# Performance work log

Hardware: AMD Instinct MI355X
Metric: run time of the kernel (lower is better)

Reference implementation:

```python
import jax, jax.numpy as jnp
import numpy as np

DIM = 1024
N_HEADS = 16
HEAD_DIM = DIM // N_HEADS
B, T = 2, 2048


def get_rotary_embedding(T, head_dim, dtype=jnp.float32):
    inv_freq = 1.0 / (10000.0 ** (jnp.arange(0, head_dim, 2, dtype=jnp.float32) / head_dim))
    t = jnp.arange(T, dtype=jnp.float32)
    freqs = jnp.einsum('t,f->tf', t, inv_freq)          # [T, head_dim/2]
    emb = jnp.concatenate([freqs, freqs], axis=-1)       # [T, head_dim]
    return jnp.sin(emb).astype(dtype), jnp.cos(emb).astype(dtype)


def rotate_half(x):
    x1, x2 = jnp.split(x, 2, axis=-1)
    return jnp.concatenate([-x2, x1], axis=-1)


def apply_rotary_pos_emb(x, sin, cos):
    # x: [B, H, T, D]; sin/cos: [T, D] broadcast over B, H
    return x * cos + rotate_half(x) * sin


def setup_inputs() -> dict:
    key = jax.random.key(0)
    ks = jax.random.split(key, 4)
    s = DIM ** -0.5
    return {
        'x': jax.random.normal(ks[0], (B, T, DIM), jnp.float32),
        'W_qkv': jax.random.normal(ks[1], (DIM, 3 * DIM), jnp.float32) * s,
        'b_qkv': jnp.zeros((3 * DIM,), jnp.float32),
        'W_out': jax.random.normal(ks[2], (DIM, DIM), jnp.float32) * s,
        'b_out': jnp.zeros((DIM,), jnp.float32),
    }


def reference(x, W_qkv, b_qkv, W_out, b_out):
    Bc, Tc, C = x.shape
    scale = HEAD_DIM ** -0.5
    qkv = x @ W_qkv + b_qkv                                    # [B, T, 3C]
    qkv = qkv.reshape(Bc, Tc, 3, N_HEADS, HEAD_DIM)
    qkv = jnp.transpose(qkv, (2, 0, 3, 1, 4))                  # [3, B, H, T, D]
    q, k, v = qkv[0], qkv[1], qkv[2]
    sin, cos = get_rotary_embedding(Tc, HEAD_DIM, x.dtype)
    q = apply_rotary_pos_emb(q, sin, cos)
    k = apply_rotary_pos_emb(k, sin, cos)
    attn = jnp.einsum('bhqd,bhkd->bhqk', q, k) * scale         # [B, H, T, T]
    probs = jax.nn.softmax(attn, axis=-1)
    out = jnp.einsum('bhqk,bhkd->bhqd', probs, v)              # [B, H, T, D]
    out = jnp.transpose(out, (0, 2, 1, 3)).reshape(Bc, Tc, C)
    return out @ W_out + b_out
```

## Files before the change

### kernel.cpp

```cpp
#include <hip/hip_runtime.h>
#include <hip/hip_bf16.h>
#include <cstdint>
#include <cstddef>

typedef unsigned short ushort_t;
typedef __bf16 bf16x8 __attribute__((ext_vector_type(8)));
typedef float f32x4 __attribute__((ext_vector_type(4)));

#define DEV static __device__ __forceinline__

DEV void gl2lds16(const void* g, void* l) {
  __builtin_amdgcn_global_load_lds(
      (const __attribute__((address_space(1))) void*)(uintptr_t)g,
      (__attribute__((address_space(3))) void*)(uintptr_t)l, 16, 0, 0);
}

DEV bf16x8 ldfrag(const void* p) { return __builtin_bit_cast(bf16x8, *(const uint4*)p); }

DEV f32x4 mfma16(bf16x8 a, bf16x8 b, f32x4 c) {
  return __builtin_amdgcn_mfma_f32_16x16x32_bf16(a, b, c, 0, 0, 0);
}

DEV ushort_t f2b(float f) { return __builtin_bit_cast(ushort_t, __float2bfloat16(f)); }
DEV unsigned int cvtpk(float lo, float hi) {
  unsigned int r;
  asm("v_cvt_pk_bf16_f32 %0, %1, %2" : "=v"(r) : "v"(lo), "v"(hi));
  return r;
}

__global__ __launch_bounds__(256) void k_cast_bf16(const float* __restrict__ X,
                                                   ushort_t* __restrict__ Y, int n) {
  int i = (blockIdx.x * 256 + threadIdx.x) * 4;
  if (i >= n) return;
  float4 v = *(const float4*)(X + i);
  ushort4 o;
  o.x = f2b(v.x); o.y = f2b(v.y); o.z = f2b(v.z); o.w = f2b(v.w);
  *(ushort4*)(Y + i) = o;
}

__global__ __launch_bounds__(256) void k_castT(const float* __restrict__ W,
                                               ushort_t* __restrict__ WT, int K, int N) {
  __shared__ ushort_t tile[64][72];
  int n0 = blockIdx.x * 64, k0 = blockIdx.y * 64;
  int t = threadIdx.x;
#pragma unroll
  for (int i = 0; i < 16; ++i) {
    int e = i * 256 + t; int r = e >> 6, c = e & 63;
    tile[c][r] = f2b(W[(size_t)(k0 + r) * N + n0 + c]);
  }
  __syncthreads();
#pragma unroll
  for (int i = 0; i < 16; ++i) {
    int e = i * 256 + t; int rn = e >> 6, ck = e & 63;
    WT[(size_t)(n0 + rn) * K + k0 + ck] = tile[rn][ck];
  }
}

__global__ __launch_bounds__(256) void k_rope_table(float* __restrict__ sintab,
                                                    float* __restrict__ costab) {
  int id = blockIdx.x * 256 + threadIdx.x;
  int f = id & 31, t = id >> 5;
  float invf = exp2f(-(float)f * 0.4152410118609203f);
  float ang = (float)t * invf;
  sintab[id] = sinf(ang);
  costab[id] = cosf(ang);
}

template <int EPI, int BM, int BN>
__global__ __launch_bounds__(256, 2) void k_gemm_bt(
    const ushort_t* __restrict__ A, const ushort_t* __restrict__ BT,
    const float* __restrict__ bias, ushort_t* __restrict__ Oq,
    ushort_t* __restrict__ Ok, ushort_t* __restrict__ Ov,
    float* __restrict__ Of, const float* __restrict__ sintab,
    const float* __restrict__ costab, int K, int N) {
  constexpr int MI = BM / 32, NJ = BN / 32;
  __shared__ __align__(16) char As[2][BM * 64];
  __shared__ __align__(16) char Bs[2][BN * 64];
  const int tid = threadIdx.x, lane = tid & 63, wv = tid >> 6;
  const int l15 = lane & 15, l4 = lane >> 4;
  const int nt = blockIdx.x, mt = blockIdx.y;
  const char* Ab = (const char*)(A + (size_t)mt * BM * K);
  const char* Bb = (const char*)(BT + (size_t)nt * BN * K);
  const int rs = K * 2;
  const int wr = (wv >> 1) * (BM / 2), wc = (wv & 1) * (BN / 2);
  f32x4 acc[MI][NJ] = {};
#pragma unroll
  for (int ii = 0; ii < BM / 64; ++ii) {
    int slot = wv * (BM / 64) + ii;
    int r = slot * 16 + (lane >> 2);
    int scb = ((lane & 3) * 16) ^ ((r & 3) << 4);
    gl2lds16(Ab + (size_t)r * rs + scb, As[0] + slot * 1024);
  }
#pragma unroll
  for (int ii = 0; ii < BN / 64; ++ii) {
    int slot = wv * (BN / 64) + ii;
    int r = slot * 16 + (lane >> 2);
    int scb = ((lane & 3) * 16) ^ ((r & 3) << 4);
    gl2lds16(Bb + (size_t)r * rs + scb, Bs[0] + slot * 1024);
  }
  __syncthreads();
  for (int k0 = 0; k0 < K; k0 += 32) {
    const int cur = (k0 >> 5) & 1;
    if (k0 + 32 < K) {
#pragma unroll
      for (int ii = 0; ii < BM / 64; ++ii) {
        int slot = wv * (BM / 64) + ii;
        int r = slot * 16 + (lane >> 2);
        int scb = ((lane & 3) * 16) ^ ((r & 3) << 4);
        gl2lds16(Ab + (size_t)r * rs + (k0 + 32) * 2 + scb, As[cur ^ 1] + slot * 1024);
      }
#pragma unroll
      for (int ii = 0; ii < BN / 64; ++ii) {
        int slot = wv * (BN / 64) + ii;
        int r = slot * 16 + (lane >> 2);
        int scb = ((lane & 3) * 16) ^ ((r & 3) << 4);
        gl2lds16(Bb + (size_t)r * rs + (k0 + 32) * 2 + scb, Bs[cur ^ 1] + slot * 1024);
      }
    }
    bf16x8 af[MI], bg[NJ];
#pragma unroll
    for (int i = 0; i < MI; ++i) {
      int r = wr + i * 16 + l15;
      af[i] = ldfrag(As[cur] + r * 64 + ((l4 * 16) ^ ((r & 3) << 4)));
    }
#pragma unroll
    for (int j = 0; j < NJ; ++j) {
      int r = wc + j * 16 + l15;
      bg[j] = ldfrag(Bs[cur] + r * 64 + ((l4 * 16) ^ ((r & 3) << 4)));
    }
    __builtin_amdgcn_s_setprio(1);
#pragma unroll
    for (int i = 0; i < MI; ++i)
#pragma unroll
      for (int j = 0; j < NJ; ++j)
        acc[i][j] = mfma16(af[i], bg[j], acc[i][j]);
    __builtin_amdgcn_s_setprio(0);
    __syncthreads();
  }
  if constexpr (EPI == 0) {
    const int colbase = nt * BN + wc;
    const int part = colbase >> 10;
    const int h = (colbase >> 6) & 15;
    float bv[NJ];
#pragma unroll
    for (int j = 0; j < NJ; ++j) bv[j] = bias[colbase + j * 16 + l15];
    if (part <= 1) {
      ushort_t* dst = part ? Ok : Oq;
      const float sc = part ? 1.0f : 0.18033688011112042f;
#pragma unroll
      for (int i = 0; i < MI; ++i) {
        int m0 = mt * BM + wr + i * 16 + l4 * 4;
#pragma unroll
        for (int e = 0; e < 4; ++e) {
          int row = m0 + e;
          int bb = row >> 11, t = row & 2047;
          size_t rb = ((size_t)(bb * 16 + h) * 2048 + t) * 64;
#pragma unroll
          for (int j = 0; j < 2; ++j) {
            int f = j * 16 + l15;
            float x1 = acc[i][j][e] + bv[j];
            float x2 = acc[i][j + 2][e] + bv[j + 2];
            float sn = sintab[t * 32 + f], cs = costab[t * 32 + f];
            dst[rb + f]      = f2b((x1 * cs - x2 * sn) * sc);
            dst[rb + f + 32] = f2b((x2 * cs + x1 * sn) * sc);
          }
        }
      }
    } else {
#pragma unroll
      for (int i = 0; i < MI; ++i) {
        int m0 = mt * BM + wr + i * 16 + l4 * 4;
        int bb = m0 >> 11, t0 = m0 & 2047;
#pragma unroll
        for (int j = 0; j < NJ; ++j) {
          int d = j * 16 + l15;
          ushort4 pk;
          pk.x = f2b(acc[i][j][0] + bv[j]);
          pk.y = f2b(acc[i][j][1] + bv[j]);
          pk.z = f2b(acc[i][j][2] + bv[j]);
          pk.w = f2b(acc[i][j][3] + bv[j]);
          *(ushort4*)(Ov + ((size_t)(bb * 16 + h) * 64 + d) * 2048 + t0) = pk;
        }
      }
    }
  } else {
#pragma unroll
    for (int j = 0; j < NJ; ++j) {
      int c = nt * BN + wc + j * 16 + l15;
      float bvv = bias[c];
#pragma unroll
      for (int i = 0; i < MI; ++i) {
        int m0 = mt * BM + wr + i * 16 + l4 * 4;
#pragma unroll
        for (int e = 0; e < 4; ++e)
          Of[(size_t)(m0 + e) * N + c] = acc[i][j][e] + bvv;
      }
    }
  }
}

__global__ __launch_bounds__(256, 2) void k_attn(const ushort_t* __restrict__ Q,
                                                 const ushort_t* __restrict__ K,
                                                 const ushort_t* __restrict__ VT,
                                                 ushort_t* __restrict__ AO) {
  __shared__ __align__(16) char Kt[2][8192];
  __shared__ __align__(16) char Vt[2][8192];
  __shared__ __align__(16) char Pl[4][4096];
  const int tid = threadIdx.x, lane = tid & 63, wv = tid >> 6;
  const int l15 = lane & 15, l4 = lane >> 4;
  const int bh = blockIdx.x, qt = blockIdx.y;
  const int qbase = qt * 128 + wv * 32;

  const char* Qb = (const char*)(Q + ((size_t)bh * 2048 + qbase) * 64);
  bf16x8 bq[2][2];
#pragma unroll
  for (int qh = 0; qh < 2; ++qh)
#pragma unroll
    for (int c = 0; c < 2; ++c)
      bq[qh][c] = ldfrag(Qb + (qh * 16 + l15) * 128 + c * 64 + l4 * 16);

  const char* Kbase = (const char*)(K + (size_t)bh * 2048 * 64);
  const char* Vbase = (const char*)(VT + (size_t)bh * 64 * 2048);
  char* Pw = Pl[wv];

  const int sr = lane >> 3;
  const int scb = ((lane & 7) * 16) ^ ((sr & 7) << 4);

  const f32x4 mInit = {-16.f, -16.f, -16.f, -16.f};
  f32x4 ps4[2] = {};
  f32x4 o[2][4] = {};

#pragma unroll
  for (int ii = 0; ii < 2; ++ii) {
    int slot = wv * 2 + ii;
    int r = slot * 8 + sr;
    gl2lds16(Kbase + (size_t)r * 128 + scb, Kt[0] + slot * 1024);
    gl2lds16(Vbase + (size_t)r * 4096 + scb, Vt[0] + slot * 1024);
  }
  __syncthreads();

  for (int kt = 0; kt < 32; ++kt) {
    const int cur = kt & 1;
    if (kt < 31) {
#pragma unroll
      for (int ii = 0; ii < 2; ++ii) {
        int slot = wv * 2 + ii;
        int r = slot * 8 + sr;
        gl2lds16(Kbase + ((size_t)((kt + 1) * 64 + r)) * 128 + scb, Kt[cur ^ 1] + slot * 1024);
        gl2lds16(Vbase + (size_t)r * 4096 + (kt + 1) * 128 + scb, Vt[cur ^ 1] + slot * 1024);
      }
    }
    const char* Kb = Kt[cur];
    const char* Vb = Vt[cur];
    const int sw = (l15 & 7) << 4;

    f32x4 s[2][4];
    __builtin_amdgcn_s_setprio(1);
#pragma unroll
    for (int j = 0; j < 4; ++j) {
      int r = j * 16 + l15;
      bf16x8 k0 = ldfrag(Kb + r * 128 + ((l4 * 16) ^ sw));
      bf16x8 k1 = ldfrag(Kb + r * 128 + ((64 + l4 * 16) ^ sw));
#pragma unroll
      for (int qh = 0; qh < 2; ++qh) {
        f32x4 z = mfma16(k0, bq[qh][0], mInit);
        s[qh][j] = mfma16(k1, bq[qh][1], z);
      }
    }
    __builtin_amdgcn_s_setprio(0);

#pragma unroll
    for (int qh = 0; qh < 2; ++qh) {
#pragma unroll
      for (int j = 0; j < 4; ++j) {
        f32x4 p;
#pragma unroll
        for (int e = 0; e < 4; ++e) p[e] = exp2f(s[qh][j][e]);
        ps4[qh] += p;
        uint2 w;
        w.x = cvtpk(p[0], p[1]);
        w.y = cvtpk(p[2], p[3]);
        *(uint2*)(Pw + (qh * 16 + l15) * 128 + ((j * 32 + l4 * 8) ^ sw)) = w;
      }
    }

    __builtin_amdgcn_s_setprio(1);
#pragma unroll
    for (int c = 0; c < 2; ++c) {
      bf16x8 bp[2];
#pragma unroll
      for (int qh = 0; qh < 2; ++qh)
        bp[qh] = ldfrag(Pw + (qh * 16 + l15) * 128 + ((c * 64 + l4 * 16) ^ sw));
#pragma unroll
      for (int dt = 0; dt < 4; ++dt) {
        int r = dt * 16 + l15;
        bf16x8 av = ldfrag(Vb + r * 128 + ((c * 64 + l4 * 16) ^ sw));
#pragma unroll
        for (int qh = 0; qh < 2; ++qh) o[qh][dt] = mfma16(av, bp[qh], o[qh][dt]);
      }
    }
    __builtin_amdgcn_s_setprio(0);
    __syncthreads();
  }

  const int b = bh >> 4, h = bh & 15;
#pragma unroll
  for (int qh = 0; qh < 2; ++qh) {
    float t = (ps4[qh][0] + ps4[qh][1]) + (ps4[qh][2] + ps4[qh][3]);
    t += __shfl_xor(t, 16);
    t += __shfl_xor(t, 32);
    float inv = 1.0f / t;
    int q = qbase + qh * 16 + l15;
    ushort_t* dst = AO + ((size_t)(b * 2048 + q)) * 1024 + h * 64;
#pragma unroll
    for (int dt = 0; dt < 4; ++dt) {
      ushort4 pk;
      pk.x = f2b(o[qh][dt][0] * inv);
      pk.y = f2b(o[qh][dt][1] * inv);
      pk.z = f2b(o[qh][dt][2] * inv);
      pk.w = f2b(o[qh][dt][3] * inv);
      *(ushort4*)(dst + dt * 16 + l4 * 4) = pk;
    }
  }
}

extern "C" void kernel_launch(void* const* d_in, const int* in_sizes, int n_in,
                              void* d_out, int out_size, void* d_ws, size_t ws_size,
                              hipStream_t stream) {
  (void)in_sizes; (void)n_in; (void)out_size;
  const float* x    = (const float*)d_in[0];
  const float* Wqkv = (const float*)d_in[1];
  const float* bqkv = (const float*)d_in[2];
  const float* Wout = (const float*)d_in[3];
  const float* bout = (const float*)d_in[4];
  float* out = (float*)d_out;
  char* ws = (char*)d_ws;

  ushort_t* X16 = (ushort_t*)(ws + 0);
  ushort_t* WQT = (ushort_t*)(ws + 8388608);
  ushort_t* WOT = (ushort_t*)(ws + 14680064);
  ushort_t* QB  = (ushort_t*)(ws + 16777216);
  ushort_t* KB  = (ushort_t*)(ws + 25165824);
  ushort_t* VTT = (ushort_t*)(ws + 33554432);
  float* SINT   = (float*)(ws + 41943040);
  float* COST   = SINT + 65536;
  ushort_t* AO  = X16;

  if (ws_size < (size_t)42467328) return;

  k_cast_bf16<<<4096, 256, 0, stream>>>(x, X16, 4194304);
  k_castT<<<dim3(48, 16), 256, 0, stream>>>(Wqkv, WQT, 1024, 3072);
  k_castT<<<dim3(16, 16), 256, 0, stream>>>(Wout, WOT, 1024, 1024);
  k_rope_table<<<256, 256, 0, stream>>>(SINT, COST);
  k_gemm_bt<0, 128, 128><<<dim3(24, 32), 256, 0, stream>>>(
      X16, WQT, bqkv, QB, KB, VTT, nullptr, SINT, COST, 1024, 3072);
  k_attn<<<dim3(32, 16), 256, 0, stream>>>(QB, KB, VTT, AO);
  k_gemm_bt<1, 64, 128><<<dim3(8, 64), 256, 0, stream>>>(
      AO, WOT, bout, nullptr, nullptr, nullptr, out, nullptr, nullptr, 1024, 1024);
}
```

Baseline: 130.6 us.

## Merge prep kernels, remap attention blocks, and pad P tile in LDS

Merges the x cast, both weight cast-transposes and the rope table into one launch, cutting three kernel launches. The attention grid is remapped so that blocks running together are spread across different batch-heads and q-tiles, aiming to improve L2/XCD locality. The P staging buffer now uses a 136-byte padded row with two 8-byte reads instead of an XOR swizzle, changing the LDS bank-conflict pattern but possibly splitting each 16-byte read into two instructions.

```diff
diff --git a/kernel.cpp b/kernel.cpp
--- a/kernel.cpp
+++ b/kernel.cpp
@@ -16,6 +16,14 @@
 }
 
 DEV bf16x8 ldfrag(const void* p) { return __builtin_bit_cast(bf16x8, *(const uint4*)p); }
+
+DEV bf16x8 ldb64pair(const void* p) {
+  uint2 lo = *(const uint2*)p;
+  uint2 hi = *(const uint2*)((const char*)p + 8);
+  union { unsigned int u[4]; bf16x8 v; } x;
+  x.u[0] = lo.x; x.u[1] = lo.y; x.u[2] = hi.x; x.u[3] = hi.y;
+  return x.v;
+}
 
 DEV f32x4 mfma16(bf16x8 a, bf16x8 b, f32x4 c) {
   return __builtin_amdgcn_mfma_f32_16x16x32_bf16(a, b, c, 0, 0, 0);
@@ -28,40 +36,46 @@
   return r;
 }
 
-__global__ __launch_bounds__(256) void k_cast_bf16(const float* __restrict__ X,
-                                                   ushort_t* __restrict__ Y, int n) {
-  int i = (blockIdx.x * 256 + threadIdx.x) * 4;
-  if (i >= n) return;
-  float4 v = *(const float4*)(X + i);
-  ushort4 o;
-  o.x = f2b(v.x); o.y = f2b(v.y); o.z = f2b(v.z); o.w = f2b(v.w);
-  *(ushort4*)(Y + i) = o;
-}
-
-__global__ __launch_bounds__(256) void k_castT(const float* __restrict__ W,
-                                               ushort_t* __restrict__ WT, int K, int N) {
+__global__ __launch_bounds__(256) void k_prep(const float* __restrict__ x,
+                                              const float* __restrict__ Wqkv,
+                                              const float* __restrict__ Wout,
+                                              ushort_t* __restrict__ X16,
+                                              ushort_t* __restrict__ WQT,
+                                              ushort_t* __restrict__ WOT,
+                                              float* __restrict__ sintab,
+                                              float* __restrict__ costab) {
   __shared__ ushort_t tile[64][72];
-  int n0 = blockIdx.x * 64, k0 = blockIdx.y * 64;
-  int t = threadIdx.x;
-#pragma unroll
-  for (int i = 0; i < 16; ++i) {
-    int e = i * 256 + t; int r = e >> 6, c = e & 63;
-    tile[c][r] = f2b(W[(size_t)(k0 + r) * N + n0 + c]);
-  }
-  __syncthreads();
-#pragma unroll
-  for (int i = 0; i < 16; ++i) {
-    int e = i * 256 + t; int rn = e >> 6, ck = e & 63;
-    WT[(size_t)(n0 + rn) * K + k0 + ck] = tile[rn][ck];
-  }
-}
-
-__global__ __launch_bounds__(256) void k_rope_table(float* __restrict__ sintab,
-                                                    float* __restrict__ costab) {
-  int id = blockIdx.x * 256 + threadIdx.x;
-  int f = id & 31, t = id >> 5;
+  const int b = blockIdx.x, t = threadIdx.x;
+  if (b < 4096) {
+    int i = (b * 256 + t) * 4;
+    float4 v = *(const float4*)(x + i);
+    ushort4 o;
+    o.x = f2b(v.x); o.y = f2b(v.y); o.z = f2b(v.z); o.w = f2b(v.w);
+    *(ushort4*)(X16 + i) = o;
+    return;
+  }
+  if (b < 5120) {
+    const float* W; ushort_t* WT; int N, bb, Nb;
+    if (b < 4864) { W = Wqkv; WT = WQT; N = 3072; bb = b - 4096; Nb = 48; }
+    else          { W = Wout; WT = WOT; N = 1024; bb = b - 4864; Nb = 16; }
+    const int n0 = (bb % Nb) * 64, k0 = (bb / Nb) * 64, K = 1024;
+#pragma unroll
+    for (int i = 0; i < 16; ++i) {
+      int e = i * 256 + t; int r = e >> 6, c = e & 63;
+      tile[c][r] = f2b(W[(size_t)(k0 + r) * N + n0 + c]);
+    }
+    __syncthreads();
+#pragma unroll
+    for (int i = 0; i < 16; ++i) {
+      int e = i * 256 + t; int rn = e >> 6, ck = e & 63;
+      WT[(size_t)(n0 + rn) * K + k0 + ck] = tile[rn][ck];
+    }
+    return;
+  }
+  int id = (b - 5120) * 256 + t;
+  int f = id & 31, tt = id >> 5;
   float invf = exp2f(-(float)f * 0.4152410118609203f);
-  float ang = (float)t * invf;
+  float ang = (float)tt * invf;
   sintab[id] = sinf(ang);
   costab[id] = cosf(ang);
 }
@@ -205,10 +219,12 @@
                                                  ushort_t* __restrict__ AO) {
   __shared__ __align__(16) char Kt[2][8192];
   __shared__ __align__(16) char Vt[2][8192];
-  __shared__ __align__(16) char Pl[4][4096];
+  __shared__ __align__(16) char Pl[4][4352];
   const int tid = threadIdx.x, lane = tid & 63, wv = tid >> 6;
   const int l15 = lane & 15, l4 = lane >> 4;
-  const int bh = blockIdx.x, qt = blockIdx.y;
+  const int lin = blockIdx.x + (blockIdx.y << 4);
+  const int nl = ((lin & 7) << 6) + (lin >> 3);
+  const int qt = nl & 15, bh = nl >> 4;
   const int qbase = qt * 128 + wv * 32;
 
   const char* Qb = (const char*)(Q + ((size_t)bh * 2048 + qbase) * 64);
@@ -280,7 +296,7 @@
         uint2 w;
         w.x = cvtpk(p[0], p[1]);
         w.y = cvtpk(p[2], p[3]);
-        *(uint2*)(Pw + (qh * 16 + l15) * 128 + ((j * 32 + l4 * 8) ^ sw)) = w;
+        *(uint2*)(Pw + (qh * 16 + l15) * 136 + j * 32 + l4 * 8) = w;
       }
     }
 
@@ -290,7 +306,7 @@
       bf16x8 bp[2];
 #pragma unroll
       for (int qh = 0; qh < 2; ++qh)
-        bp[qh] = ldfrag(Pw + (qh * 16 + l15) * 128 + ((c * 64 + l4 * 16) ^ sw));
+        bp[qh] = ldb64pair(Pw + (qh * 16 + l15) * 136 + c * 64 + l4 * 16);
 #pragma unroll
       for (int dt = 0; dt < 4; ++dt) {
         int r = dt * 16 + l15;
@@ -348,13 +364,10 @@
 
   if (ws_size < (size_t)42467328) return;
 
-  k_cast_bf16<<<4096, 256, 0, stream>>>(x, X16, 4194304);
-  k_castT<<<dim3(48, 16), 256, 0, stream>>>(Wqkv, WQT, 1024, 3072);
-  k_castT<<<dim3(16, 16), 256, 0, stream>>>(Wout, WOT, 1024, 1024);
-  k_rope_table<<<256, 256, 0, stream>>>(SINT, COST);
+  k_prep<<<5376, 256, 0, stream>>>(x, Wqkv, Wout, X16, WQT, WOT, SINT, COST);
   k_gemm_bt<0, 128, 128><<<dim3(24, 32), 256, 0, stream>>>(
       X16, WQT, bqkv, QB, KB, VTT, nullptr, SINT, COST, 1024, 3072);
-  k_attn<<<dim3(32, 16), 256, 0, stream>>>(QB, KB, VTT, AO);
+  k_attn<<<dim3(16, 32), 256, 0, stream>>>(QB, KB, VTT, AO);
   k_gemm_bt<1, 64, 128><<<dim3(8, 64), 256, 0, stream>>>(
       AO, WOT, bout, nullptr, nullptr, nullptr, out, nullptr, nullptr, 1024, 1024);
 }
```

Measured after the change: 125.5 us. 3.9% less time.
